# Kernel tuning notes

Measured on AMD Instinct MI355X. Metric: run time of the kernel, lower is better.

## Reference

```python
import jax, jax.numpy as jnp
from jax import lax
import numpy as np

ROI = 7  # roi_size


def _extract_rois(feat, coords):
    """Faithful port of extract_roi_features: clamp a 7x7 window to image bounds,
    then bilinearly resize the (possibly smaller) crop back to 7x7
    (F.interpolate, mode='bilinear', align_corners=False)."""
    B, C, H, W = feat.shape
    half = ROI // 2

    def axis_idx(c, size):
        start = jnp.maximum(0, c - half)                  # [B,A]
        end = jnp.minimum(size, c + half + 1)
        Li = end - start                                  # crop length (int) [B,A]
        L = Li.astype(feat.dtype)[..., None]              # [B,A,1]
        j = jnp.arange(ROI, dtype=feat.dtype)
        # align_corners=False source coordinate, clamped into the crop
        src = jnp.clip((j + 0.5) * L / ROI - 0.5, 0.0, L - 1.0)  # [B,A,7]
        i0 = jnp.floor(src).astype(jnp.int32)
        i1 = jnp.minimum(i0 + 1, Li[..., None] - 1)
        w1 = src - i0.astype(feat.dtype)
        return start[..., None] + i0, start[..., None] + i1, 1.0 - w1, w1

    xc = coords[..., 0].astype(jnp.int32)
    yc = coords[..., 1].astype(jnp.int32)
    y0, y1, wy0, wy1 = axis_idx(yc, H)
    x0, x1, wx0, wx1 = axis_idx(xc, W)
    Bn, A = xc.shape
    bi = jnp.arange(Bn)[:, None, None, None]

    def g(Y, X):  # gather -> [B,A,7,7,C]
        return feat[bi, :, Y[:, :, :, None], X[:, :, None, :]]

    wy0 = wy0[:, :, :, None, None]; wy1 = wy1[:, :, :, None, None]
    wx0 = wx0[:, :, None, :, None]; wx1 = wx1[:, :, None, :, None]
    v = (wy0 * wx0 * g(y0, x0) + wy0 * wx1 * g(y0, x1)
         + wy1 * wx0 * g(y1, x0) + wy1 * wx1 * g(y1, x1))
    return jnp.transpose(v, (0, 1, 4, 2, 3))  # [B,A,C,7,7]


def _conv(x, w, b, pad):
    y = lax.conv_general_dilated(x, w, (1, 1), [(pad, pad), (pad, pad)],
                                 dimension_numbers=('NCHW', 'OIHW', 'NCHW'))
    return y + b[None, :, None, None]


def _bn(x, scale, bias, mean, var, eps=1e-5):
    inv = scale * lax.rsqrt(var + eps)
    return x * inv[None, :, None, None] + (bias - mean * inv)[None, :, None, None]


def setup_inputs() -> dict:
    key = jax.random.key(0)
    ks = jax.random.split(key, 12)
    B, A, C, H, W = 8, 128, 256, 64, 64
    f32 = jnp.float32
    d = {}
    d['feat_rgb'] = jax.random.normal(ks[0], (B, C, H, W), f32)
    d['feat_tir'] = jax.random.normal(ks[1], (B, C, H, W), f32)
    d['anchor_coords'] = jax.random.randint(ks[2], (B, A, 2), 0, 64).astype(jnp.int32)
    # local_fusion: Conv(2C->C,3) BN ReLU Conv(C->C,3) BN ReLU
    d['conv1_w'] = jax.random.normal(ks[3], (C, 2 * C, 3, 3), f32) * 0.02
    d['conv1_b'] = jnp.zeros((C,), f32)
    d['bn1_scale'] = jnp.ones((C,), f32)
    d['bn1_bias'] = jnp.zeros((C,), f32)
    d['bn1_mean'] = jax.random.normal(ks[4], (C,), f32) * 0.1
    d['bn1_var'] = jax.random.uniform(ks[5], (C,), f32, 0.5, 1.5)
    d['conv2_w'] = jax.random.normal(ks[6], (C, C, 3, 3), f32) * 0.02
    d['conv2_b'] = jnp.zeros((C,), f32)
    d['bn2_scale'] = jnp.ones((C,), f32)
    d['bn2_bias'] = jnp.zeros((C,), f32)
    d['bn2_mean'] = jax.random.normal(ks[7], (C,), f32) * 0.1
    d['bn2_var'] = jax.random.uniform(ks[8], (C,), f32, 0.5, 1.5)
    # weight_generator: Conv(C->C//4,1) ReLU Conv(C//4->2,1) Softmax(dim=1)
    d['wg1_w'] = jax.random.normal(ks[9], (C // 4, C, 1, 1), f32) * 0.05
    d['wg1_b'] = jnp.zeros((C // 4,), f32)
    d['wg2_w'] = jax.random.normal(ks[10], (2, C // 4, 1, 1), f32) * 0.05
    d['wg2_b'] = jnp.zeros((2,), f32)
    return d


def reference(feat_rgb, feat_tir, anchor_coords,
              conv1_w, conv1_b, bn1_scale, bn1_bias, bn1_mean, bn1_var,
              conv2_w, conv2_b, bn2_scale, bn2_bias, bn2_mean, bn2_var,
              wg1_w, wg1_b, wg2_w, wg2_b):
    B, C, H, W = feat_rgb.shape
    A = anchor_coords.shape[1]
    roi_rgb = _extract_rois(feat_rgb, anchor_coords)  # [B,A,C,7,7]
    roi_tir = _extract_rois(feat_tir, anchor_coords)
    rgb = roi_rgb.reshape(B * A, C, ROI, ROI)
    tir = roi_tir.reshape(B * A, C, ROI, ROI)
    x = jnp.concatenate([rgb, tir], axis=1)           # [B*A, 2C, 7, 7]
    x = jax.nn.relu(_bn(_conv(x, conv1_w, conv1_b, 1), bn1_scale, bn1_bias, bn1_mean, bn1_var))
    x = jax.nn.relu(_bn(_conv(x, conv2_w, conv2_b, 1), bn2_scale, bn2_bias, bn2_mean, bn2_var))
    h = jax.nn.relu(_conv(x, wg1_w, wg1_b, 0))
    w = jax.nn.softmax(_conv(h, wg2_w, wg2_b, 0), axis=1)  # [B*A, 2, 7, 7]
    fused = w[:, 0:1] * rgb + w[:, 1:2] * tir
    return fused.reshape(B, A, C, ROI, ROI)
```

## Files before the change

### kernel.cpp

```cpp
#include <hip/hip_runtime.h>
#include <cstddef>
#include <cstdint>


typedef unsigned int u32;
typedef unsigned short u16;
typedef __attribute__((ext_vector_type(8))) short short8;
typedef __attribute__((ext_vector_type(16))) float float16v;

__device__ __forceinline__ float bf2f(u16 u) {
  u32 x = ((u32)u) << 16;
  return __builtin_bit_cast(float, x);
}
__device__ __forceinline__ u16 f2bf(float f) {
  u32 x = __builtin_bit_cast(u32, f);
  x = x + 0x7fffu + ((x >> 16) & 1u);
  return (u16)(x >> 16);
}
__device__ __forceinline__ void gl_lds16(const void* g, void* l) {
  __builtin_amdgcn_global_load_lds((const __attribute__((address_space(1))) void*)g,
                                   (__attribute__((address_space(3))) void*)l, 16, 0, 0);
}

template <int IC>
__global__ void k_prep_w(const float* __restrict__ w, u16* __restrict__ wt) {
  int i = blockIdx.x * 256 + threadIdx.x;
  if (i >= 9 * 256 * IC) return;
  int e = i & 7;
  int r = i >> 3;
  int oc = r & 255;
  int r2 = r >> 8;
  int oct = r2 % (IC / 8);
  int t = r2 / (IC / 8);
  int ic = oct * 8 + e;
  wt[i] = f2bf(w[((size_t)oc * IC + ic) * 9 + t]);
}

__global__ void k_prep_bn(const float* __restrict__ cb, const float* __restrict__ sc,
                          const float* __restrict__ bi, const float* __restrict__ mn,
                          const float* __restrict__ vr, float* __restrict__ sb) {
  int c = threadIdx.x;
  float inv = sc[c] * rsqrtf(vr[c] + 1e-5f);
  sb[c]       = inv;
  sb[256 + c] = cb[c] * inv + (bi[c] - mn[c] * inv);
}

__global__ __launch_bounds__(256)
void k_roi2(const float* __restrict__ frgb, const float* __restrict__ ftir,
            const int* __restrict__ coords, u16* __restrict__ cat) {
  int ba = blockIdx.x, b = ba >> 7, tid = threadIdx.x;
  __shared__ int   si0[2][7], si1[2][7];
  __shared__ float sw0[2][7], sw1[2][7];
  __shared__ u16 tile[49][514];
  if (tid < 14) {
    int axis = tid / 7;
    int j = tid - axis * 7;
    int c = coords[ba * 2 + (axis == 0 ? 1 : 0)];
    int start = max(0, c - 3);
    int end   = min(64, c + 4);
    int Li = end - start;
    float L = (float)Li;
    float src = ((float)j + 0.5f) * L / 7.0f - 0.5f;
    src = fminf(fmaxf(src, 0.0f), L - 1.0f);
    int i0 = (int)floorf(src);
    int i1 = min(i0 + 1, Li - 1);
    float w1 = src - (float)i0;
    si0[axis][j] = start + i0;
    si1[axis][j] = start + i1;
    sw0[axis][j] = 1.0f - w1;
    sw1[axis][j] = w1;
  }
  __syncthreads();
  const float* fr = frgb + (size_t)b * 256 * 4096;
  const float* ft = ftir + (size_t)b * 256 * 4096;
  for (int idx = tid; idx < 256 * 49; idx += 256) {
    int c = idx / 49, p = idx - c * 49;
    int jy = p / 7, jx = p - (p / 7) * 7;
    int y0 = si0[0][jy], y1 = si1[0][jy];
    int x0 = si0[1][jx], x1 = si1[1][jx];
    float wy0 = sw0[0][jy], wy1 = sw1[0][jy];
    float wx0 = sw0[1][jx], wx1 = sw1[1][jx];
    float a00 = wy0 * wx0, a01 = wy0 * wx1, a10 = wy1 * wx0, a11 = wy1 * wx1;
    const float* fc = fr + (size_t)c * 4096;
    float vr_ = a00 * fc[y0 * 64 + x0] + a01 * fc[y0 * 64 + x1] +
                a10 * fc[y1 * 64 + x0] + a11 * fc[y1 * 64 + x1];
    const float* gc = ft + (size_t)c * 4096;
    float vt_ = a00 * gc[y0 * 64 + x0] + a01 * gc[y0 * 64 + x1] +
                a10 * gc[y1 * 64 + x0] + a11 * gc[y1 * 64 + x1];
    tile[p][c]       = f2bf(vr_);
    tile[p][256 + c] = f2bf(vt_);
  }
  __syncthreads();
  u16* dst = cat + (size_t)ba * 49 * 512;
  for (int o = tid; o < 49 * 512; o += 256) {
    int row = o >> 9, c = o & 511;
    dst[o] = tile[row][c];
  }
}

template <int ICT, bool FIRST>
__global__ __launch_bounds__(1024, 4)
void k_conv_mfma(const u16* __restrict__ IN, const u16* __restrict__ WT,
                 const float* __restrict__ sb, u16* __restrict__ OUT) {
  constexpr int NC = ICT / 64;
  constexpr int BUFB = 200 * 128;
  __shared__ __align__(16) u16 lds[2][BUFB / 2];
  const int tid = threadIdx.x;
  const int lane = tid & 63, wv = tid >> 6;
  const int ng = wv & 3, mg = wv >> 2;
  const int l31 = lane & 31, h32 = lane >> 5;
  const int ba4 = blockIdx.x * 4;
  const char* inb = (const char*)IN;
  const bool dead1 = (mg == 3);

  if (tid < 64) {
    short8 zz = (short8){0, 0, 0, 0, 0, 0, 0, 0};
    int buf = tid >> 5, idx = tid & 31;
    *(short8*)((char*)&lds[buf][0] + 196 * 128 + idx * 16) = zz;
  }
  __syncthreads();

  int base_[2], qy_[2], qx_[2];
#pragma unroll
  for (int i = 0; i < 2; ++i) {
    int P = (mg + 4 * i) * 32 + l31;
    if (P > 195) P = 195;
    int roi = P / 49;
    int q = P - roi * 49;
    base_[i] = roi * 49;
    qy_[i] = q / 7;
    qx_[i] = q - (q / 7) * 7;
  }

  float16v acc[2][2];
#pragma unroll
  for (int i = 0; i < 2; ++i)
#pragma unroll
    for (int f = 0; f < 2; ++f)
#pragma unroll
      for (int e = 0; e < 16; ++e) acc[i][f][e] = 0.0f;

  auto stage = [&](int ch, int buf) {
    int cl = ((lane & 7) * 16) ^ (((lane >> 3) & 7) << 4);
    for (int s = wv; s < 25; s += 16) {
      if (s < 24 || lane < 32) {
        const char* src = inb +
            ((size_t)(ba4 * 49 + s * 8 + (lane >> 3))) * (ICT * 2) + ch * 128 + cl;
        gl_lds16(src, (char*)&lds[buf][0] + s * 1024);
      }
    }
  };

  stage(0, 0);
  __syncthreads();

  const u16* wthr = WT + (size_t)h32 * 2048 + (size_t)(ng * 64 + l31) * 8;

  int cur = 0;
#pragma unroll 1
  for (int ch = 0; ch < NC; ++ch) {
    if (ch + 1 < NC) stage(ch + 1, cur ^ 1);
    const char* lb = (const char*)&lds[cur][0];
    const u16* wch = wthr + (size_t)ch * 8 * 2048;

    short8 wfr[3][2];
#pragma unroll
    for (int jp = 0; jp < 2; ++jp)
#pragma unroll
      for (int f = 0; f < 2; ++f)
        wfr[jp][f] = *(const short8*)(
            wch + (size_t)(jp * 2) * 2048 + f * 256);
    int row0 = 0, row1 = 0;
#pragma unroll
    for (int j = 0; j < 36; ++j) {
      const int t = j >> 2, kk = j & 3;
      if (kk == 0) {
        const int dy = t / 3 - 1, dx = t - (t / 3) * 3 - 1;
#pragma unroll
        for (int i = 0; i < 2; ++i) {
          int iy = qy_[i] + dy, ix = qx_[i] + dx;
          int ok = ((u32)iy < 7u) & ((u32)ix < 7u);
          int row = ok ? (base_[i] + iy * 7 + ix) : 196;
          if (i == 0) row0 = row; else row1 = row;
        }
      }
      if (j + 2 < 36) {
        const int jn = j + 2;
#pragma unroll
        for (int f = 0; f < 2; ++f)
          wfr[jn % 3][f] = *(const short8*)(
              wch + (size_t)((jn >> 2) * (ICT / 8) + (jn & 3) * 2) * 2048 + f * 256);
      }
      short8 bfr[2];
      {
        int byt0 = row0 * 128 + ((kk * 32 + h32 * 16) ^ ((row0 & 7) << 4));
        bfr[0] = *(const short8*)(lb + byt0);
      }
      if (!dead1) {
        int byt1 = row1 * 128 + ((kk * 32 + h32 * 16) ^ ((row1 & 7) << 4));
        bfr[1] = *(const short8*)(lb + byt1);
      }
      __builtin_amdgcn_s_setprio(1);
#pragma unroll
      for (int i = 0; i < 2; ++i) {
        if (i == 1 && dead1) continue;
#pragma unroll
        for (int f = 0; f < 2; ++f)
          acc[i][f] = FIRST
              ? __builtin_amdgcn_mfma_f32_32x32x16_bf16(bfr[i], wfr[j % 3][f],
                                                        acc[i][f], 0, 0, 0)
              : __builtin_amdgcn_mfma_f32_32x32x16_bf16(wfr[j % 3][f], bfr[i],
                                                        acc[i][f], 0, 0, 0);
      }
      __builtin_amdgcn_s_setprio(0);
    }
    __syncthreads();
    cur ^= 1;
  }

  if (FIRST) {
    u16* ob = OUT + (size_t)ba4 * 49 * 256;
#pragma unroll
    for (int f = 0; f < 2; ++f) {
      int oc = ng * 64 + f * 32 + l31;
      float s = sb[oc], bb = sb[256 + oc];
#pragma unroll
      for (int i = 0; i < 2; ++i) {
        if (i == 1 && dead1) continue;
        int ti = mg + 4 * i;
#pragma unroll
        for (int reg = 0; reg < 16; ++reg) {
          int m = (reg & 3) + 8 * (reg >> 2) + 4 * h32;
          int P = ti * 32 + m;
          if (P < 196)
            ob[(size_t)P * 256 + oc] = f2bf(fmaxf(acc[i][f][reg] * s + bb, 0.0f));
        }
      }
    }
  } else {
#pragma unroll
    for (int i = 0; i < 2; ++i) {
      if (i == 1 && dead1) continue;
      int ti = mg + 4 * i;
      int P = ti * 32 + l31;
      if (P < 196) {
        int roi = P / 49;
        int q = P - roi * 49;
        u16* ob = OUT + ((size_t)(ba4 + roi) * 256) * 49 + q;
#pragma unroll
        for (int f = 0; f < 2; ++f)
#pragma unroll
          for (int reg = 0; reg < 16; ++reg) {
            int oc = ng * 64 + f * 32 + (reg & 3) + 8 * (reg >> 2) + 4 * h32;
            float s = sb[oc], bb = sb[256 + oc];
            ob[(size_t)oc * 49] = f2bf(fmaxf(acc[i][f][reg] * s + bb, 0.0f));
          }
      }
    }
  }
}

__global__ __launch_bounds__(256)
void k_head_fuse(const u16* __restrict__ x3, const u16* __restrict__ cat,
                 const float* __restrict__ w1, const float* __restrict__ b1,
                 const float* __restrict__ w2, const float* __restrict__ b2,
                 float* __restrict__ out) {
  int ba  = blockIdx.x;
  int tid = threadIdx.x;
  __shared__ float xs[256 * 49];
  __shared__ float hs[64 * 49];
  __shared__ float ls[2 * 49];
  __shared__ float swx[2 * 49];
  const u16* src = x3 + (size_t)ba * 256 * 49;
  for (int idx = tid; idx < 256 * 49; idx += 256) xs[idx] = bf2f(src[idx]);
  __syncthreads();
  for (int idx = tid; idx < 64 * 49; idx += 256) {
    int oh = idx / 49, p = idx - oh * 49;
    float s = b1[oh];
    const float* wr = w1 + oh * 256;
    for (int ic = 0; ic < 256; ++ic) s += wr[ic] * xs[ic * 49 + p];
    hs[idx] = fmaxf(s, 0.0f);
  }
  __syncthreads();
  if (tid < 98) {
    int chn = tid / 49, p = tid - chn * 49;
    float s = b2[chn];
    const float* wr = w2 + chn * 64;
    for (int k = 0; k < 64; ++k) s += wr[k] * hs[k * 49 + p];
    ls[tid] = s;
  }
  __syncthreads();
  if (tid < 49) {
    float l0 = ls[tid], l1 = ls[49 + tid];
    float m = fmaxf(l0, l1);
    float e0 = expf(l0 - m), e1 = expf(l1 - m);
    float d = e0 + e1;
    swx[tid]      = e0 / d;
    swx[49 + tid] = e1 / d;
  }
  __syncthreads();
  const u16* cr = cat + (size_t)ba * 49 * 512;
  float* o = out + (size_t)ba * 256 * 49;
  for (int idx = tid; idx < 256 * 49; idx += 256) {
    int c = idx / 49, p = idx - (idx / 49) * 49;
    float rgb = bf2f(cr[p * 512 + c]);
    float tir = bf2f(cr[p * 512 + 256 + c]);
    o[idx] = swx[p] * rgb + swx[49 + p] * tir;
  }
}

extern "C" void kernel_launch(void* const* d_in, const int* in_sizes, int n_in,
                              void* d_out, int out_size, void* d_ws, size_t ws_size,
                              hipStream_t stream) {
  const float* feat_rgb = (const float*)d_in[0];
  const float* feat_tir = (const float*)d_in[1];
  const int*   coords   = (const int*)d_in[2];
  const float* conv1_w  = (const float*)d_in[3];
  const float* conv1_b  = (const float*)d_in[4];
  const float* bn1_s    = (const float*)d_in[5];
  const float* bn1_b    = (const float*)d_in[6];
  const float* bn1_m    = (const float*)d_in[7];
  const float* bn1_v    = (const float*)d_in[8];
  const float* conv2_w  = (const float*)d_in[9];
  const float* conv2_b  = (const float*)d_in[10];
  const float* bn2_s    = (const float*)d_in[11];
  const float* bn2_b    = (const float*)d_in[12];
  const float* bn2_m    = (const float*)d_in[13];
  const float* bn2_v    = (const float*)d_in[14];
  const float* wg1_w    = (const float*)d_in[15];
  const float* wg1_b    = (const float*)d_in[16];
  const float* wg2_w    = (const float*)d_in[17];
  const float* wg2_b    = (const float*)d_in[18];
  float* out = (float*)d_out;

  char* base = (char*)d_ws;
  u16*   W1T  = (u16*)(base);
  u16*   W2T  = (u16*)(base + 2359296);
  float* SB1  = (float*)(base + 2359296 + 1179648);
  float* SB2  = (float*)(base + 2359296 + 1179648 + 2048);
  u16*   CAT  = (u16*)(base + 3543040);
  u16*   X2   = (u16*)(base + 3543040 + 51380224);
  u16*   X3   = (u16*)(base + 3543040 + 51380224 + 25690112);

  k_prep_w<512><<<(9 * 256 * 512 + 255) / 256, 256, 0, stream>>>(conv1_w, W1T);
  k_prep_w<256><<<(9 * 256 * 256 + 255) / 256, 256, 0, stream>>>(conv2_w, W2T);
  k_prep_bn<<<1, 256, 0, stream>>>(conv1_b, bn1_s, bn1_b, bn1_m, bn1_v, SB1);
  k_prep_bn<<<1, 256, 0, stream>>>(conv2_b, bn2_s, bn2_b, bn2_m, bn2_v, SB2);
  k_roi2<<<1024, 256, 0, stream>>>(feat_rgb, feat_tir, coords, CAT);
  k_conv_mfma<512, true><<<256, 1024, 0, stream>>>(CAT, W1T, SB1, X2);
  k_conv_mfma<256, false><<<256, 1024, 0, stream>>>(X2, W2T, SB2, X3);
  k_head_fuse<<<1024, 256, 0, stream>>>(X3, CAT, wg1_w, wg1_b, wg2_w, wg2_b, out);
}
```

Baseline: 656.1 us.

## Remap conv MFMA waves to own 32 channels across all seven pixel tiles

The conv kernel goes from 16 waves per block, each covering a 2x2 slice of M-tiles by N-fragments, to 8 waves per block, each owning 32 output channels and all 7 pixel tiles. Each weight fragment loaded from global memory now feeds 7 MFMAs instead of up to 4, and the wave that previously idled on a dead tile is gone. The cost is 7 accumulators plus 7 B-fragment reads per step, so register pressure rises, and each block has half as many waves to hide LDS and global latency.

```diff
diff --git a/kernel.cpp b/kernel.cpp
--- a/kernel.cpp
+++ b/kernel.cpp
@@ -99,7 +99,7 @@
 }
 
 template <int ICT, bool FIRST>
-__global__ __launch_bounds__(1024, 4)
+__global__ __launch_bounds__(512, 2)
 void k_conv_mfma(const u16* __restrict__ IN, const u16* __restrict__ WT,
                  const float* __restrict__ sb, u16* __restrict__ OUT) {
   constexpr int NC = ICT / 64;
@@ -107,11 +107,9 @@
   __shared__ __align__(16) u16 lds[2][BUFB / 2];
   const int tid = threadIdx.x;
   const int lane = tid & 63, wv = tid >> 6;
-  const int ng = wv & 3, mg = wv >> 2;
   const int l31 = lane & 31, h32 = lane >> 5;
   const int ba4 = blockIdx.x * 4;
   const char* inb = (const char*)IN;
-  const bool dead1 = (mg == 3);
 
   if (tid < 64) {
     short8 zz = (short8){0, 0, 0, 0, 0, 0, 0, 0};
@@ -120,10 +118,10 @@
   }
   __syncthreads();
 
-  int base_[2], qy_[2], qx_[2];
-#pragma unroll
-  for (int i = 0; i < 2; ++i) {
-    int P = (mg + 4 * i) * 32 + l31;
+  int base_[7], qy_[7], qx_[7];
+#pragma unroll
+  for (int i = 0; i < 7; ++i) {
+    int P = i * 32 + l31;
     if (P > 195) P = 195;
     int roi = P / 49;
     int q = P - roi * 49;
@@ -132,17 +130,15 @@
     qx_[i] = q - (q / 7) * 7;
   }
 
-  float16v acc[2][2];
-#pragma unroll
-  for (int i = 0; i < 2; ++i)
-#pragma unroll
-    for (int f = 0; f < 2; ++f)
-#pragma unroll
-      for (int e = 0; e < 16; ++e) acc[i][f][e] = 0.0f;
+  float16v acc[7];
+#pragma unroll
+  for (int i = 0; i < 7; ++i)
+#pragma unroll
+    for (int e = 0; e < 16; ++e) acc[i][e] = 0.0f;
 
   auto stage = [&](int ch, int buf) {
     int cl = ((lane & 7) * 16) ^ (((lane >> 3) & 7) << 4);
-    for (int s = wv; s < 25; s += 16) {
+    for (int s = wv; s < 25; s += 8) {
       if (s < 24 || lane < 32) {
         const char* src = inb +
             ((size_t)(ba4 * 49 + s * 8 + (lane >> 3))) * (ICT * 2) + ch * 128 + cl;
@@ -154,7 +150,7 @@
   stage(0, 0);
   __syncthreads();
 
-  const u16* wthr = WT + (size_t)h32 * 2048 + (size_t)(ng * 64 + l31) * 8;
+  const u16* wthr = WT + (size_t)h32 * 2048 + (size_t)(wv * 32 + l31) * 8;
 
   int cur = 0;
 #pragma unroll 1
@@ -163,55 +159,42 @@
     const char* lb = (const char*)&lds[cur][0];
     const u16* wch = wthr + (size_t)ch * 8 * 2048;
 
-    short8 wfr[3][2];
+    short8 wfr[3];
 #pragma unroll
     for (int jp = 0; jp < 2; ++jp)
-#pragma unroll
-      for (int f = 0; f < 2; ++f)
-        wfr[jp][f] = *(const short8*)(
-            wch + (size_t)(jp * 2) * 2048 + f * 256);
-    int row0 = 0, row1 = 0;
+      wfr[jp] = *(const short8*)(wch + (size_t)(jp * 2) * 2048);
+    int row_[7];
 #pragma unroll
     for (int j = 0; j < 36; ++j) {
       const int t = j >> 2, kk = j & 3;
       if (kk == 0) {
         const int dy = t / 3 - 1, dx = t - (t / 3) * 3 - 1;
 #pragma unroll
-        for (int i = 0; i < 2; ++i) {
+        for (int i = 0; i < 7; ++i) {
           int iy = qy_[i] + dy, ix = qx_[i] + dx;
           int ok = ((u32)iy < 7u) & ((u32)ix < 7u);
-          int row = ok ? (base_[i] + iy * 7 + ix) : 196;
-          if (i == 0) row0 = row; else row1 = row;
+          row_[i] = ok ? (base_[i] + iy * 7 + ix) : 196;
         }
       }
       if (j + 2 < 36) {
         const int jn = j + 2;
-#pragma unroll
-        for (int f = 0; f < 2; ++f)
-          wfr[jn % 3][f] = *(const short8*)(
-              wch + (size_t)((jn >> 2) * (ICT / 8) + (jn & 3) * 2) * 2048 + f * 256);
-      }
-      short8 bfr[2];
-      {
-        int byt0 = row0 * 128 + ((kk * 32 + h32 * 16) ^ ((row0 & 7) << 4));
-        bfr[0] = *(const short8*)(lb + byt0);
-      }
-      if (!dead1) {
-        int byt1 = row1 * 128 + ((kk * 32 + h32 * 16) ^ ((row1 & 7) << 4));
-        bfr[1] = *(const short8*)(lb + byt1);
+        wfr[jn % 3] = *(const short8*)(
+            wch + (size_t)((jn >> 2) * (ICT / 8) + (jn & 3) * 2) * 2048);
+      }
+      short8 bfr[7];
+#pragma unroll
+      for (int i = 0; i < 7; ++i) {
+        int byt = row_[i] * 128 + ((kk * 32 + h32 * 16) ^ ((row_[i] & 7) << 4));
+        bfr[i] = *(const short8*)(lb + byt);
       }
       __builtin_amdgcn_s_setprio(1);
 #pragma unroll
-      for (int i = 0; i < 2; ++i) {
-        if (i == 1 && dead1) continue;
-#pragma unroll
-        for (int f = 0; f < 2; ++f)
-          acc[i][f] = FIRST
-              ? __builtin_amdgcn_mfma_f32_32x32x16_bf16(bfr[i], wfr[j % 3][f],
-                                                        acc[i][f], 0, 0, 0)
-              : __builtin_amdgcn_mfma_f32_32x32x16_bf16(wfr[j % 3][f], bfr[i],
-                                                        acc[i][f], 0, 0, 0);
-      }
+      for (int i = 0; i < 7; ++i)
+        acc[i] = FIRST
+            ? __builtin_amdgcn_mfma_f32_32x32x16_bf16(bfr[i], wfr[j % 3],
+                                                      acc[i], 0, 0, 0)
+            : __builtin_amdgcn_mfma_f32_32x32x16_bf16(wfr[j % 3], bfr[i],
+                                                      acc[i], 0, 0, 0);
       __builtin_amdgcn_s_setprio(0);
     }
     __syncthreads();
@@ -220,41 +203,31 @@
 
   if (FIRST) {
     u16* ob = OUT + (size_t)ba4 * 49 * 256;
-#pragma unroll
-    for (int f = 0; f < 2; ++f) {
-      int oc = ng * 64 + f * 32 + l31;
-      float s = sb[oc], bb = sb[256 + oc];
-#pragma unroll
-      for (int i = 0; i < 2; ++i) {
-        if (i == 1 && dead1) continue;
-        int ti = mg + 4 * i;
-#pragma unroll
-        for (int reg = 0; reg < 16; ++reg) {
-          int m = (reg & 3) + 8 * (reg >> 2) + 4 * h32;
-          int P = ti * 32 + m;
-          if (P < 196)
-            ob[(size_t)P * 256 + oc] = f2bf(fmaxf(acc[i][f][reg] * s + bb, 0.0f));
-        }
-      }
-    }
+    int oc = wv * 32 + l31;
+    float s = sb[oc], bb = sb[256 + oc];
+#pragma unroll
+    for (int i = 0; i < 7; ++i)
+#pragma unroll
+      for (int reg = 0; reg < 16; ++reg) {
+        int m = (reg & 3) + 8 * (reg >> 2) + 4 * h32;
+        int P = i * 32 + m;
+        if (P < 196)
+          ob[(size_t)P * 256 + oc] = f2bf(fmaxf(acc[i][reg] * s + bb, 0.0f));
+      }
   } else {
 #pragma unroll
-    for (int i = 0; i < 2; ++i) {
-      if (i == 1 && dead1) continue;
-      int ti = mg + 4 * i;
-      int P = ti * 32 + l31;
+    for (int i = 0; i < 7; ++i) {
+      int P = i * 32 + l31;
       if (P < 196) {
         int roi = P / 49;
         int q = P - roi * 49;
         u16* ob = OUT + ((size_t)(ba4 + roi) * 256) * 49 + q;
 #pragma unroll
-        for (int f = 0; f < 2; ++f)
-#pragma unroll
-          for (int reg = 0; reg < 16; ++reg) {
-            int oc = ng * 64 + f * 32 + (reg & 3) + 8 * (reg >> 2) + 4 * h32;
-            float s = sb[oc], bb = sb[256 + oc];
-            ob[(size_t)oc * 49] = f2bf(fmaxf(acc[i][f][reg] * s + bb, 0.0f));
-          }
+        for (int reg = 0; reg < 16; ++reg) {
+          int oc = wv * 32 + (reg & 3) + 8 * (reg >> 2) + 4 * h32;
+          float s = sb[oc], bb = sb[256 + oc];
+          ob[(size_t)oc * 49] = f2bf(fmaxf(acc[i][reg] * s + bb, 0.0f));
+        }
       }
     }
   }
@@ -347,7 +320,7 @@
   k_prep_bn<<<1, 256, 0, stream>>>(conv1_b, bn1_s, bn1_b, bn1_m, bn1_v, SB1);
   k_prep_bn<<<1, 256, 0, stream>>>(conv2_b, bn2_s, bn2_b, bn2_m, bn2_v, SB2);
   k_roi2<<<1024, 256, 0, stream>>>(feat_rgb, feat_tir, coords, CAT);
-  k_conv_mfma<512, true><<<256, 1024, 0, stream>>>(CAT, W1T, SB1, X2);
-  k_conv_mfma<256, false><<<256, 1024, 0, stream>>>(X2, W2T, SB2, X3);
+  k_conv_mfma<512, true><<<256, 512, 0, stream>>>(CAT, W1T, SB1, X2);
+  k_conv_mfma<256, false><<<256, 512, 0, stream>>>(X2, W2T, SB2, X3);
   k_head_fuse<<<1024, 256, 0, stream>>>(X3, CAT, wg1_w, wg1_b, wg2_w, wg2_b, out);
 }
```

Result: slower. 925.2 us (+41.0%).

## Triple-buffer conv LDS staging with vmcnt waits and global zero-pad rows

Applied to the files above, without the earlier changes.

The conv kernel's input staging moves from double to triple buffering in LDS, so two chunks are prefetched ahead. The per-chunk __syncthreads becomes an explicit s_waitcnt vmcnt plus s_barrier, so the load two chunks ahead can stay in flight. Zero padding rows are now fetched through the same global-to-LDS load path from a zeroed workspace buffer, replacing the separate LDS zero-init and its barrier. The cost is more LDS per block, which may reduce how many blocks fit on a CU, and hand-managed wait counts that must match the number of loads issued.

```diff
diff --git a/kernel.cpp b/kernel.cpp
--- a/kernel.cpp
+++ b/kernel.cpp
@@ -38,11 +38,14 @@
 
 __global__ void k_prep_bn(const float* __restrict__ cb, const float* __restrict__ sc,
                           const float* __restrict__ bi, const float* __restrict__ mn,
-                          const float* __restrict__ vr, float* __restrict__ sb) {
+                          const float* __restrict__ vr, float* __restrict__ sb,
+                          float* __restrict__ zp) {
   int c = threadIdx.x;
   float inv = sc[c] * rsqrtf(vr[c] + 1e-5f);
   sb[c]       = inv;
   sb[256 + c] = cb[c] * inv + (bi[c] - mn[c] * inv);
+  zp[c] = 0.0f;
+  zp[256 + c] = 0.0f;
 }
 
 __global__ __launch_bounds__(256)
@@ -101,24 +104,19 @@
 template <int ICT, bool FIRST>
 __global__ __launch_bounds__(1024, 4)
 void k_conv_mfma(const u16* __restrict__ IN, const u16* __restrict__ WT,
-                 const float* __restrict__ sb, u16* __restrict__ OUT) {
+                 const float* __restrict__ sb, const float* __restrict__ zpad,
+                 u16* __restrict__ OUT) {
   constexpr int NC = ICT / 64;
-  constexpr int BUFB = 200 * 128;
-  __shared__ __align__(16) u16 lds[2][BUFB / 2];
+  constexpr int BUFB = 208 * 128;
+  __shared__ __align__(16) u16 lds[3][BUFB / 2];
   const int tid = threadIdx.x;
   const int lane = tid & 63, wv = tid >> 6;
   const int ng = wv & 3, mg = wv >> 2;
   const int l31 = lane & 31, h32 = lane >> 5;
   const int ba4 = blockIdx.x * 4;
   const char* inb = (const char*)IN;
+  const char* zpb = (const char*)zpad;
   const bool dead1 = (mg == 3);
-
-  if (tid < 64) {
-    short8 zz = (short8){0, 0, 0, 0, 0, 0, 0, 0};
-    int buf = tid >> 5, idx = tid & 31;
-    *(short8*)((char*)&lds[buf][0] + 196 * 128 + idx * 16) = zz;
-  }
-  __syncthreads();
 
   int base_[2], qy_[2], qx_[2];
 #pragma unroll
@@ -142,25 +140,31 @@
 
   auto stage = [&](int ch, int buf) {
     int cl = ((lane & 7) * 16) ^ (((lane >> 3) & 7) << 4);
-    for (int s = wv; s < 25; s += 16) {
-      if (s < 24 || lane < 32) {
-        const char* src = inb +
-            ((size_t)(ba4 * 49 + s * 8 + (lane >> 3))) * (ICT * 2) + ch * 128 + cl;
-        gl_lds16(src, (char*)&lds[buf][0] + s * 1024);
-      }
+#pragma unroll
+    for (int u = 0; u < 2; ++u) {
+      int s = wv + u * 16;
+      int soff = (s <= 24) ? s * 1024 : 25 * 1024;
+      int row_g = s * 8 + (lane >> 3);
+      const char* src = (row_g < 196)
+          ? (inb + ((size_t)(ba4 * 49 + row_g)) * (ICT * 2) + ch * 128 + cl)
+          : (zpb + cl);
+      gl_lds16(src, (char*)&lds[buf][0] + soff);
     }
   };
 
+  const u16* wthr = WT + (size_t)h32 * 2048 + (size_t)(ng * 64 + l31) * 8;
+
   stage(0, 0);
-  __syncthreads();
-
-  const u16* wthr = WT + (size_t)h32 * 2048 + (size_t)(ng * 64 + l31) * 8;
-
-  int cur = 0;
+  stage(1, 1);
+  asm volatile("s_waitcnt vmcnt(2)" ::: "memory");
+  __builtin_amdgcn_sched_barrier(0);
+  __builtin_amdgcn_s_barrier();
+  __builtin_amdgcn_sched_barrier(0);
+
 #pragma unroll 1
   for (int ch = 0; ch < NC; ++ch) {
-    if (ch + 1 < NC) stage(ch + 1, cur ^ 1);
-    const char* lb = (const char*)&lds[cur][0];
+    if (ch + 2 < NC) stage(ch + 2, (ch + 2) % 3);
+    const char* lb = (const char*)&lds[ch % 3][0];
     const u16* wch = wthr + (size_t)ch * 8 * 2048;
 
     short8 wfr[3][2];
@@ -214,8 +218,15 @@
       }
       __builtin_amdgcn_s_setprio(0);
     }
-    __syncthreads();
-    cur ^= 1;
+
+    if (ch + 2 < NC) {
+      asm volatile("s_waitcnt vmcnt(2)" ::: "memory");
+    } else {
+      asm volatile("s_waitcnt vmcnt(0)" ::: "memory");
+    }
+    __builtin_amdgcn_sched_barrier(0);
+    __builtin_amdgcn_s_barrier();
+    __builtin_amdgcn_sched_barrier(0);
   }
 
   if (FIRST) {
@@ -336,18 +347,19 @@
   char* base = (char*)d_ws;
   u16*   W1T  = (u16*)(base);
   u16*   W2T  = (u16*)(base + 2359296);
-  float* SB1  = (float*)(base + 2359296 + 1179648);
-  float* SB2  = (float*)(base + 2359296 + 1179648 + 2048);
-  u16*   CAT  = (u16*)(base + 3543040);
-  u16*   X2   = (u16*)(base + 3543040 + 51380224);
-  u16*   X3   = (u16*)(base + 3543040 + 51380224 + 25690112);
+  float* SB1  = (float*)(base + 3538944);
+  float* SB2  = (float*)(base + 3540992);
+  float* ZPAD = (float*)(base + 3543040);
+  u16*   CAT  = (u16*)(base + 3545088);
+  u16*   X2   = (u16*)(base + 3545088 + 51380224);
+  u16*   X3   = (u16*)(base + 3545088 + 51380224 + 25690112);
 
   k_prep_w<512><<<(9 * 256 * 512 + 255) / 256, 256, 0, stream>>>(conv1_w, W1T);
   k_prep_w<256><<<(9 * 256 * 256 + 255) / 256, 256, 0, stream>>>(conv2_w, W2T);
-  k_prep_bn<<<1, 256, 0, stream>>>(conv1_b, bn1_s, bn1_b, bn1_m, bn1_v, SB1);
-  k_prep_bn<<<1, 256, 0, stream>>>(conv2_b, bn2_s, bn2_b, bn2_m, bn2_v, SB2);
+  k_prep_bn<<<1, 256, 0, stream>>>(conv1_b, bn1_s, bn1_b, bn1_m, bn1_v, SB1, ZPAD);
+  k_prep_bn<<<1, 256, 0, stream>>>(conv2_b, bn2_s, bn2_b, bn2_m, bn2_v, SB2, ZPAD);
   k_roi2<<<1024, 256, 0, stream>>>(feat_rgb, feat_tir, coords, CAT);
-  k_conv_mfma<512, true><<<256, 1024, 0, stream>>>(CAT, W1T, SB1, X2);
-  k_conv_mfma<256, false><<<256, 1024, 0, stream>>>(X2, W2T, SB2, X3);
+  k_conv_mfma<512, true><<<256, 1024, 0, stream>>>(CAT, W1T, SB1, ZPAD, X2);
+  k_conv_mfma<256, false><<<256, 1024, 0, stream>>>(X2, W2T, SB2, ZPAD, X3);
   k_head_fuse<<<1024, 256, 0, stream>>>(X3, CAT, wg1_w, wg1_b, wg2_w, wg2_b, out);
 }
```

Result: slower. 674.0 us (+2.7%).
